# Optimization experiments

Hardware: AMD Instinct MI355X
Metric: run time of the kernel (lower is better)

Reference implementation:

```python
import jax, jax.numpy as jnp
import numpy as np

N = 50000   # nodes
E = 800000  # edges (avg degree 16)
F = 128     # input_nf = output_nf
H = 128     # hidden_nf


def setup_inputs() -> dict:
    key = jax.random.key(0)
    ks = jax.random.split(key, 10)
    # coords: spatial part in [-1, 1], z-coordinate (last dim) in [0.5, 1.5] (must be > 0)
    xz = jax.random.uniform(ks[0], (N, 3), minval=-1.0, maxval=1.0)
    xz = xz.at[:, -1].set(jax.random.uniform(ks[1], (N,), minval=0.5, maxval=1.5))
    h = jax.random.normal(ks[2], (N, F), dtype=jnp.float32)
    row = jax.random.randint(ks[3], (E,), 0, N)
    # guarantee col != row so AdS distance is strictly positive on every edge
    col = (row + 1 + jax.random.randint(ks[4], (E,), 0, N - 1)) % N
    edge_index = jnp.stack([row, col]).astype(jnp.int32)

    def lin(k, fan_in, fan_out):
        return jax.random.normal(k, (fan_in, fan_out), dtype=jnp.float32) / np.float32(np.sqrt(fan_in))

    return {
        "xz": xz,
        "h": h,
        "We1": lin(ks[5], 2 * F + 1, H), "be1": jnp.full((H,), 0.1, jnp.float32),
        "We2": lin(ks[6], H, H),         "be2": jnp.full((H,), 0.1, jnp.float32),
        "Wn1": lin(ks[7], H + F, H),     "bn1": jnp.full((H,), 0.1, jnp.float32),
        "Wn2": lin(ks[8], H, F),         "bn2": jnp.full((F,), 0.1, jnp.float32),
        "edge_index": edge_index,
    }


def reference(xz, h, We1, be1, We2, be2, Wn1, bn1, Wn2, bn2, edge_index):
    row, col = edge_index[0], edge_index[1]
    n = h.shape[0]

    # AdS (hyperbolic upper-half-space) distance between xz[row] and xz[col]:
    # d = arccosh(1 + |p1 - p2|^2 / (2 z1 z2)), z = last coordinate
    diff = xz[row] - xz[col]                                  # [E, 3]
    u = jnp.sum(diff * diff, axis=-1) / (2.0 * xz[row, -1] * xz[col, -1])
    dist = jnp.arccosh(1.0 + u)[:, None]                      # [E, 1]

    # edge model: concat(source, target, radial) -> Linear -> silu -> Linear -> silu
    m = jnp.concatenate([h[row], h[col], dist], axis=1)       # [E, 2F+1]
    m = jax.nn.silu(m @ We1 + be1)                            # [E, H]
    m = jax.nn.silu(m @ We2 + be2)                            # [E, H]

    # segment_mean over destination nodes (row)
    num = jax.ops.segment_sum(m, row, num_segments=n)                          # [N, H]
    den = jax.ops.segment_sum(jnp.ones_like(m), row, num_segments=n)          # [N, H]
    agg = num / jnp.maximum(den, jnp.ones((), den.dtype))

    # node model: concat(h, agg) -> Linear -> silu -> Linear, plus residual
    z = jnp.concatenate([h, agg], axis=1)                     # [N, F+H]
    out = jax.nn.silu(z @ Wn1 + bn1) @ Wn2 + bn2              # [N, F]
    return h + out
```

## Files before the change

### kernel.cpp

```cpp
#include <hip/hip_runtime.h>

#define NN 50000
#define EE 800000
#define NB 196

typedef __bf16 bf16x8 __attribute__((ext_vector_type(8)));
typedef float  f32x4  __attribute__((ext_vector_type(4)));

__device__ __forceinline__ float bf2f(ushort u) {
    union { unsigned int i; float f; } v; v.i = ((unsigned int)u) << 16; return v.f;
}
__device__ __forceinline__ ushort f2bf(float f) {
    union { float f; unsigned int i; } v; v.f = f;
    unsigned int u = v.i;
    return (ushort)((u + 0x7FFFu + ((u >> 16) & 1u)) >> 16);
}
__device__ __forceinline__ ushort f2bf_fast(float f) {
    union { float f; unsigned int i; } v; v.f = f;
    return (ushort)((v.i + 0x8000u) >> 16);
}
__device__ __forceinline__ float silu(float x) {
    return x * __builtin_amdgcn_rcpf(1.0f + __expf(-x));
}

__device__ __forceinline__ bool detect_isf(const ushort* __restrict__ xzu,
                                           int tid, int* scnt) {
    float v = bf2f(xzu[2 * (tid & 255)]);
    bool sane = (v == v) && (fabsf(v) <= 4.0f);
    unsigned long long m = __ballot(sane);
    if ((tid & 63) == 0) scnt[tid >> 6] = __popcll(m);
    __syncthreads();
    int cnt = scnt[0] + scnt[1] + scnt[2] + scnt[3];
    return cnt < 192;
}

__global__ void prep_all_kernel(const void* __restrict__ hsrc, const void* __restrict__ xzsrc,
                                const int* __restrict__ erow,
                                const void* We1, const void* We2,
                                const void* Wn1, const void* Wn2,
                                const void* be1, const void* be2,
                                const void* bn1, const void* bn2,
                                ushort* __restrict__ hb, float* __restrict__ xzf,
                                int* __restrict__ cntI,
                                ushort* __restrict__ We1s, ushort* __restrict__ We2s,
                                ushort* __restrict__ Wn1s, ushort* __restrict__ Wn2s,
                                float* __restrict__ fb, ushort* __restrict__ wlb) {
    __shared__ int scnt[4];
    const int b = blockIdx.x;
    const int tid = threadIdx.x;

    if (b >= 3712 && b < 6837) {
        int e = (b - 3712) * 256 + tid;
        if (e < EE) atomicAdd(&cntI[erow[e]], 1);
        return;
    }

    const bool isf = detect_isf((const ushort*)xzsrc, tid, scnt);

    if (b < 3125) {
        int i = (b * 256 + tid) * 8;
        uint4 o;
        if (isf) {
            const float* s = (const float*)hsrc + i;
            float4 f0 = *(const float4*)s;
            float4 f1 = *(const float4*)(s + 4);
            o.x = (unsigned int)f2bf(f0.x) | ((unsigned int)f2bf(f0.y) << 16);
            o.y = (unsigned int)f2bf(f0.z) | ((unsigned int)f2bf(f0.w) << 16);
            o.z = (unsigned int)f2bf(f1.x) | ((unsigned int)f2bf(f1.y) << 16);
            o.w = (unsigned int)f2bf(f1.z) | ((unsigned int)f2bf(f1.w) << 16);
        } else {
            o = *(const uint4*)((const ushort*)hsrc + i);
        }
        *(uint4*)(hb + i) = o;
    } else if (b < 3712) {
        int i = (b - 3125) * 256 + tid;
        if (i < NN * 3)
            xzf[i] = isf ? ((const float*)xzsrc)[i] : bf2f(((const ushort*)xzsrc)[i]);
    } else {
        int sw = b - 6837;
        if (sw == 48) {
            for (int j = tid; j < 640; j += 256) {
                int which = j >> 7, k = j & 127;
                const void* src = (which == 0) ? be1 : (which == 1) ? be2 :
                                  (which == 2) ? bn1 : (which == 3) ? bn2 : We1;
                size_t idx = (which == 4) ? ((size_t)256 * 128 + k) : (size_t)k;
                float v = isf ? ((const float*)src)[idx] : bf2f(((const ushort*)src)[idx]);
                fb[j] = v;
                if (which == 4) wlb[k] = f2bf(v);
            }
            return;
        }
        int c = sw * 256 + tid;
        const void* src; ushort* dst; int cl;
        if      (c <  4096) { src = We1; dst = We1s; cl = c;         }
        else if (c <  6144) { src = We2; dst = We2s; cl = c - 4096;  }
        else if (c < 10240) { src = Wn1; dst = Wn1s; cl = c - 6144;  }
        else                { src = Wn2; dst = Wn2s; cl = c - 10240; }
        int l = cl & 63, nt = (cl >> 6) & 7, kc = cl >> 9;
        int kbase = kc * 32 + (l >> 4) * 8;
        int n = nt * 16 + (l & 15);
        ushort tmp[8];
#pragma unroll
        for (int j = 0; j < 8; ++j) {
            size_t idx = (size_t)(kbase + j) * 128 + n;
            tmp[j] = isf ? f2bf(((const float*)src)[idx]) : ((const ushort*)src)[idx];
        }
#pragma unroll
        for (int j = 0; j < 8; ++j) dst[(size_t)cl * 8 + j] = tmp[j];
    }
}

__global__ void scanA_kernel(const int* __restrict__ cntI, int* __restrict__ bsum) {
    __shared__ int s[256];
    int t = threadIdx.x;
    int i = blockIdx.x * 256 + t;
    s[t] = (i < NN) ? cntI[i] : 0;
    __syncthreads();
#pragma unroll
    for (int off = 128; off > 0; off >>= 1) {
        if (t < off) s[t] += s[t + off];
        __syncthreads();
    }
    if (t == 0) bsum[blockIdx.x] = s[0];
}

__global__ void scanC_kernel(const int* __restrict__ cntI, const int* __restrict__ bsum,
                             int* __restrict__ rowStart) {
    __shared__ int s[256];
    __shared__ int sbase;
    int t = threadIdx.x;
    int bv = (t < NB) ? bsum[t] : 0;
    s[t] = bv;
    __syncthreads();
    for (int off = 1; off < 256; off <<= 1) {
        int u = (t >= off) ? s[t - off] : 0;
        __syncthreads();
        if (t >= off) s[t] += u;
        __syncthreads();
    }
    if (t == 0) sbase = (blockIdx.x == 0) ? 0 : s[blockIdx.x - 1];
    __syncthreads();
    int i = blockIdx.x * 256 + t;
    int v = (i < NN) ? cntI[i] : 0;
    s[t] = v;
    __syncthreads();
    for (int off = 1; off < 256; off <<= 1) {
        int u = (t >= off) ? s[t - off] : 0;
        __syncthreads();
        if (t >= off) s[t] += u;
        __syncthreads();
    }
    if (i < NN) rowStart[i] = sbase + s[t] - v;
}

__global__ __launch_bounds__(256, 3) void scatter_pq_kernel(
    const ushort* __restrict__ hb, const ushort* __restrict__ We1s,
    const float* __restrict__ fb, ushort* __restrict__ Pp, ushort* __restrict__ Qq,
    const int* __restrict__ erow, const int* __restrict__ ecol,
    const float* __restrict__ xzf, const int* __restrict__ rowStart,
    int* __restrict__ cursor, int4* __restrict__ eS) {
    __shared__ __align__(16) ushort sA[8192];
    const int tid = threadIdx.x;

    if (blockIdx.x >= 782) {
        int e = (blockIdx.x - 782) * 256 + tid;
        if (e >= EE) return;
        int r = erow[e], c = ecol[e];
        int pos = rowStart[r] + atomicAdd(&cursor[r], 1);
        float4 a = *(const float4*)(xzf + 3 * r);
        float4 b = *(const float4*)(xzf + 3 * c);
        float dx = a.x - b.x, dy = a.y - b.y, dz = a.z - b.z;
        float u = (dx * dx + dy * dy + dz * dz) * __builtin_amdgcn_rcpf(2.0f * a.z * b.z);
        u = fminf(fmaxf(u, 0.0f), 1.0e6f);
        float d = __logf(1.0f + u + sqrtf(u * (u + 2.0f)));
        eS[pos] = make_int4(r, c, __float_as_int(d), 0);
        return;
    }

    const int lane = tid & 63, w = tid >> 6;
    const int col = lane & 15, quad = lane >> 4;
    const int nt0 = w * 2;
    const int nA = w * 32 + col, nB = nA + 16;
    const float be1A = fb[nA], be1B = fb[nB];
    const int tile = blockIdx.x;
    const int n0 = tile * 64;
#pragma unroll
    for (int i = 0; i < 4; ++i) {
        int node = n0 + lane;
        uint4 v = (node < NN) ? *(const uint4*)(hb + (size_t)node * 128 + (w + 4 * i) * 8)
                              : make_uint4(0, 0, 0, 0);
        *(uint4*)(sA + (((lane >> 4) * 4 + i) * 64 + w * 16 + (lane & 15)) * 8) = v;
    }
    __syncthreads();

    f32x4 accP[4][2] = {}, accQ[4][2] = {};
#pragma unroll
    for (int kc = 0; kc < 4; ++kc) {
        bf16x8 bp0 = *(const bf16x8*)(We1s + ((kc * 8 + nt0)           * 64 + lane) * 8);
        bf16x8 bp1 = *(const bf16x8*)(We1s + ((kc * 8 + nt0 + 1)       * 64 + lane) * 8);
        bf16x8 bq0 = *(const bf16x8*)(We1s + (((kc + 4) * 8 + nt0)     * 64 + lane) * 8);
        bf16x8 bq1 = *(const bf16x8*)(We1s + (((kc + 4) * 8 + nt0 + 1) * 64 + lane) * 8);
#pragma unroll
        for (int g = 0; g < 4; ++g) {
            bf16x8 a = *(const bf16x8*)(sA + ((g * 4 + kc) * 64 + lane) * 8);
            accP[g][0] = __builtin_amdgcn_mfma_f32_16x16x32_bf16(a, bp0, accP[g][0], 0, 0, 0);
            accP[g][1] = __builtin_amdgcn_mfma_f32_16x16x32_bf16(a, bp1, accP[g][1], 0, 0, 0);
            accQ[g][0] = __builtin_amdgcn_mfma_f32_16x16x32_bf16(a, bq0, accQ[g][0], 0, 0, 0);
            accQ[g][1] = __builtin_amdgcn_mfma_f32_16x16x32_bf16(a, bq1, accQ[g][1], 0, 0, 0);
        }
    }
#pragma unroll
    for (int g = 0; g < 4; ++g) {
#pragma unroll
        for (int r = 0; r < 4; ++r) {
            int node = n0 + g * 16 + quad * 4 + r;
            if (node < NN) {
                size_t o = (size_t)node * 128;
                Pp[o + nA] = f2bf(accP[g][0][r] + be1A);
                Pp[o + nB] = f2bf(accP[g][1][r] + be1B);
                Qq[o + nA] = f2bf(accQ[g][0][r]);
                Qq[o + nB] = f2bf(accQ[g][1][r]);
            }
        }
    }
}

__global__ __launch_bounds__(256, 4) void edge_kernel(
    const ushort* __restrict__ Pp, const ushort* __restrict__ Qq,
    const int4* __restrict__ eS, const ushort* __restrict__ We2s,
    const ushort* __restrict__ wlb, const float* __restrict__ fb,
    float* __restrict__ agg) {
    __shared__ __align__(16) char smem[64 * 132 * 4];
    __shared__ int sRow[64];
    ushort* sM = (ushort*)smem;
    float (*sOut)[132] = (float(*)[132])smem;

    const int tid = threadIdx.x;
    const int lane = tid & 63, w = tid >> 6;
    const int col = lane & 15, quad = lane >> 4;
    const int nt0 = w * 2;

    const int nA = w * 32 + col, nB = nA + 16;
    const float be2A = fb[128 + nA], be2B = fb[128 + nB];

    const int ntiles = EE / 64;
    const int per = (ntiles + gridDim.x - 1) / gridDim.x;
    const int t0 = blockIdx.x * per;
    const int t1 = (t0 + per < ntiles) ? (t0 + per) : ntiles;
    if (t0 >= t1) return;

    bf16x8 B2[8];
#pragma unroll
    for (int kc = 0; kc < 4; ++kc) {
        B2[kc * 2]     = *(const bf16x8*)(We2s + ((kc * 8 + nt0)     * 64 + lane) * 8);
        B2[kc * 2 + 1] = *(const bf16x8*)(We2s + ((kc * 8 + nt0 + 1) * 64 + lane) * 8);
    }
    bf16x8 WL[4];
#pragma unroll
    for (int i = 0; i < 4; ++i) WL[i] = *(const bf16x8*)(wlb + (w + 4 * i) * 8);

    int4 ed = eS[(size_t)t0 * 64 + lane];

    for (int tile = t0; tile < t1; ++tile) {
        const int tn = (tile + 1 < t1) ? (tile + 1) : tile;
        const int4 edn = eS[(size_t)tn * 64 + lane];

        __syncthreads();
        const int r = ed.x, c = ed.y;
        const float d = __int_as_float(ed.z);
        if (w == 0) sRow[lane] = r;
#pragma unroll
        for (int i = 0; i < 4; ++i) {
            int ch = w + 4 * i;
            bf16x8 p = *(const bf16x8*)(Pp + (size_t)r * 128 + ch * 8);
            bf16x8 q = *(const bf16x8*)(Qq + (size_t)c * 128 + ch * 8);
            ushort out8[8];
#pragma unroll
            for (int j = 0; j < 8; ++j) {
                float x = (float)p[j] + (float)q[j] + d * (float)WL[i][j];
                out8[j] = f2bf_fast(silu(x));
            }
            *(uint4*)(sM + (((lane >> 4) * 4 + i) * 64 + w * 16 + (lane & 15)) * 8) =
                *(const uint4*)out8;
        }
        ed = edn;
        __syncthreads();

        f32x4 acc2[4][2] = {};
#pragma unroll
        for (int kc = 0; kc < 4; ++kc) {
#pragma unroll
            for (int g = 0; g < 4; ++g) {
                bf16x8 a = *(const bf16x8*)(sM + ((g * 4 + kc) * 64 + lane) * 8);
                acc2[g][0] = __builtin_amdgcn_mfma_f32_16x16x32_bf16(a, B2[kc * 2],     acc2[g][0], 0, 0, 0);
                acc2[g][1] = __builtin_amdgcn_mfma_f32_16x16x32_bf16(a, B2[kc * 2 + 1], acc2[g][1], 0, 0, 0);
            }
        }
        __syncthreads();

#pragma unroll
        for (int g = 0; g < 4; ++g) {
#pragma unroll
            for (int r4 = 0; r4 < 4; ++r4) {
                int m = g * 16 + quad * 4 + r4;
                sOut[m][nA] = silu(acc2[g][0][r4] + be2A);
                sOut[m][nB] = silu(acc2[g][1][r4] + be2B);
            }
        }
        __syncthreads();

        {
            const int cc = tid & 127;
            const int mb = (tid >> 7) * 32;
            float acc = 0.0f;
            int prow = sRow[mb];
            for (int k = 0; k < 32; ++k) {
                int rw = sRow[mb + k];
                if (rw != prow) {
                    unsafeAtomicAdd(&agg[(size_t)prow * 128 + cc], acc);
                    acc = 0.0f;
                    prow = rw;
                }
                acc += sOut[mb + k][cc];
            }
            unsafeAtomicAdd(&agg[(size_t)prow * 128 + cc], acc);
        }
    }
}

__global__ __launch_bounds__(256, 3) void node_kernel(
    const ushort* __restrict__ hb, const void* __restrict__ hraw,
    const void* __restrict__ xzsrc,
    const float* __restrict__ agg, const int* __restrict__ cntI,
    const ushort* __restrict__ Wn1s, const ushort* __restrict__ Wn2s,
    const float* __restrict__ fb, void* __restrict__ outv) {
    __shared__ __align__(16) ushort sA[16384];
    __shared__ __align__(16) ushort sM[8192];
    __shared__ int scnt[4];
    const int tid = threadIdx.x;
    const int lane = tid & 63, w = tid >> 6;
    const int col = lane & 15, quad = lane >> 4;
    const int nt0 = w * 2;
    const int ntiles = (NN + 63) / 64;
    const bool isf = detect_isf((const ushort*)xzsrc, tid, scnt);
    float* outf = (float*)outv;
    ushort* outu = (ushort*)outv;

    const int nA = w * 32 + col, nB = nA + 16;
    const float bn1A = fb[256 + nA], bn1B = fb[256 + nB];
    const float bn2A = fb[384 + nA], bn2B = fb[384 + nB];

    for (int tile = blockIdx.x; tile < ntiles; tile += gridDim.x) {
        __syncthreads();
        const int n0 = tile * 64;
#pragma unroll
        for (int i = 0; i < 8; ++i) {
            int kb = w + 4 * i;
            int node = n0 + lane;
            uint4 v;
            if (node < NN) {
                if (kb < 16) {
                    v = *(const uint4*)(hb + (size_t)node * 128 + kb * 8);
                } else {
                    const float* ap = agg + (size_t)node * 128 + (kb - 16) * 8;
                    float invc = __builtin_amdgcn_rcpf(fmaxf((float)cntI[node], 1.0f));
                    float4 f0 = *(const float4*)ap;
                    float4 f1 = *(const float4*)(ap + 4);
                    v.x = (unsigned int)f2bf_fast(f0.x * invc) | ((unsigned int)f2bf_fast(f0.y * invc) << 16);
                    v.y = (unsigned int)f2bf_fast(f0.z * invc) | ((unsigned int)f2bf_fast(f0.w * invc) << 16);
                    v.z = (unsigned int)f2bf_fast(f1.x * invc) | ((unsigned int)f2bf_fast(f1.y * invc) << 16);
                    v.w = (unsigned int)f2bf_fast(f1.z * invc) | ((unsigned int)f2bf_fast(f1.w * invc) << 16);
                }
            } else {
                v = make_uint4(0, 0, 0, 0);
            }
            *(uint4*)(sA + (((quad * 8 + i) * 64) + w * 16 + col) * 8) = v;
        }
        __syncthreads();

        f32x4 acc[4][2] = {};
#pragma unroll
        for (int kc = 0; kc < 8; ++kc) {
            bf16x8 b0 = *(const bf16x8*)(Wn1s + ((kc * 8 + nt0)     * 64 + lane) * 8);
            bf16x8 b1 = *(const bf16x8*)(Wn1s + ((kc * 8 + nt0 + 1) * 64 + lane) * 8);
#pragma unroll
            for (int g = 0; g < 4; ++g) {
                bf16x8 a = *(const bf16x8*)(sA + ((g * 8 + kc) * 64 + lane) * 8);
                acc[g][0] = __builtin_amdgcn_mfma_f32_16x16x32_bf16(a, b0, acc[g][0], 0, 0, 0);
                acc[g][1] = __builtin_amdgcn_mfma_f32_16x16x32_bf16(a, b1, acc[g][1], 0, 0, 0);
            }
        }
#pragma unroll
        for (int g = 0; g < 4; ++g) {
            int base0 = ((g * 4 + w) * 64 + (col >> 3) * 16) * 8 + (col & 7);
#pragma unroll
            for (int r = 0; r < 4; ++r) {
                int mrow = quad * 4 + r;
                sM[base0 + mrow * 8]              = f2bf_fast(silu(acc[g][0][r] + bn1A));
                sM[base0 + 2 * 16 * 8 + mrow * 8] = f2bf_fast(silu(acc[g][1][r] + bn1B));
            }
        }
        __syncthreads();

        f32x4 acc2[4][2] = {};
#pragma unroll
        for (int kc = 0; kc < 4; ++kc) {
            bf16x8 b0 = *(const bf16x8*)(Wn2s + ((kc * 8 + nt0)     * 64 + lane) * 8);
            bf16x8 b1 = *(const bf16x8*)(Wn2s + ((kc * 8 + nt0 + 1) * 64 + lane) * 8);
#pragma unroll
            for (int g = 0; g < 4; ++g) {
                bf16x8 a = *(const bf16x8*)(sM + ((g * 4 + kc) * 64 + lane) * 8);
                acc2[g][0] = __builtin_amdgcn_mfma_f32_16x16x32_bf16(a, b0, acc2[g][0], 0, 0, 0);
                acc2[g][1] = __builtin_amdgcn_mfma_f32_16x16x32_bf16(a, b1, acc2[g][1], 0, 0, 0);
            }
        }
#pragma unroll
        for (int g = 0; g < 4; ++g) {
#pragma unroll
            for (int r = 0; r < 4; ++r) {
                int ml2 = g * 16 + quad * 4 + r;
                int node = n0 + ml2;
                if (node < NN) {
                    size_t oi = (size_t)node * 128;
                    float h0 = isf ? ((const float*)hraw)[oi + nA] : bf2f(((const ushort*)hraw)[oi + nA]);
                    float h1 = isf ? ((const float*)hraw)[oi + nB] : bf2f(((const ushort*)hraw)[oi + nB]);
                    float x0 = acc2[g][0][r] + bn2A + h0;
                    float x1 = acc2[g][1][r] + bn2B + h1;
                    if (isf) { outf[oi + nA] = x0; outf[oi + nB] = x1; }
                    else     { outu[oi + nA] = f2bf_fast(x0); outu[oi + nB] = f2bf_fast(x1); }
                }
            }
        }
    }
}

extern "C" void kernel_launch(void* const* d_in, const int* in_sizes, int n_in,
                              void* d_out, int out_size, void* d_ws, size_t ws_size,
                              hipStream_t stream) {
    const void* xz  = d_in[0];
    const void* h   = d_in[1];
    const void* We1 = d_in[2];
    const void* be1 = d_in[3];
    const void* We2 = d_in[4];
    const void* be2 = d_in[5];
    const void* Wn1 = d_in[6];
    const void* bn1 = d_in[7];
    const void* Wn2 = d_in[8];
    const void* bn2 = d_in[9];
    const int*  ei  = (const int*)d_in[10];
    const int* erow = ei;
    const int* ecol = ei + EE;

    char* base = (char*)d_ws;
    size_t cur = 0;
    auto alloc = [&](size_t bytes) { size_t o = cur; cur = (cur + bytes + 255) & ~(size_t)255; return o; };
    float*  agg    = (float*) (base + alloc((size_t)NN * 128 * 4));
    int*    cntI   = (int*)   (base + alloc((size_t)NN * 4));
    int*    cursor = (int*)   (base + alloc((size_t)NN * 4));
    ushort* hb     = (ushort*)(base + alloc((size_t)NN * 128 * 2));
    ushort* Pp     = (ushort*)(base + alloc((size_t)NN * 128 * 2));
    ushort* Qq     = (ushort*)(base + alloc((size_t)NN * 128 * 2));
    int4*   eS     = (int4*)  (base + alloc((size_t)EE * 16));
    float*  xzf    = (float*) (base + alloc((size_t)NN * 3 * 4 + 16));
    int*    rowSt  = (int*)   (base + alloc((size_t)NN * 4));
    int*    bsum   = (int*)   (base + alloc(256 * 4));
    ushort* We1s   = (ushort*)(base + alloc(32768 * 2));
    ushort* We2s   = (ushort*)(base + alloc(16384 * 2));
    ushort* Wn1s   = (ushort*)(base + alloc(32768 * 2));
    ushort* Wn2s   = (ushort*)(base + alloc(16384 * 2));
    float*  fb     = (float*) (base + alloc(640 * 4));
    ushort* wlb    = (ushort*)(base + alloc(128 * 2));

    size_t zbytes = (size_t)((char*)hb - (char*)agg);
    (void)hipMemsetAsync(agg, 0, zbytes, stream);

    prep_all_kernel<<<6886, 256, 0, stream>>>(h, xz, erow, We1, We2, Wn1, Wn2,
                                              be1, be2, bn1, bn2,
                                              hb, xzf, cntI, We1s, We2s, Wn1s, Wn2s,
                                              fb, wlb);
    scanA_kernel<<<NB, 256, 0, stream>>>(cntI, bsum);
    scanC_kernel<<<NB, 256, 0, stream>>>(cntI, bsum, rowSt);
    scatter_pq_kernel<<<782 + 3125, 256, 0, stream>>>(hb, We1s, fb, Pp, Qq,
                                                      erow, ecol, xzf, rowSt, cursor, eS);
    edge_kernel<<<1024, 256, 0, stream>>>(Pp, Qq, eS, We2s, wlb, fb, agg);
    node_kernel<<<782, 256, 0, stream>>>(hb, h, xz, agg, cntI, Wn1s, Wn2s, fb, d_out);
}
```

Baseline: 331.8 us.

## Software-pipeline edge kernel with double-buffered message tile and gather prefetch

The edge kernel gets a double-buffered shared-memory tile for the first-layer activations, and the P/Q gathers for the next tile are issued before the current tile's MFMA work. Gather latency can then overlap with compute, and one barrier per tile is removed. In exchange, shared memory grows because sM and sOut no longer alias, more registers hold the prefetched data, and launch bounds drop from 4 to 2 blocks per CU, which lowers occupancy.

```diff
diff --git a/kernel.cpp b/kernel.cpp
--- a/kernel.cpp
+++ b/kernel.cpp
@@ -225,15 +225,14 @@
     }
 }
 
-__global__ __launch_bounds__(256, 4) void edge_kernel(
+__global__ __launch_bounds__(256, 2) void edge_kernel(
     const ushort* __restrict__ Pp, const ushort* __restrict__ Qq,
     const int4* __restrict__ eS, const ushort* __restrict__ We2s,
     const ushort* __restrict__ wlb, const float* __restrict__ fb,
     float* __restrict__ agg) {
-    __shared__ __align__(16) char smem[64 * 132 * 4];
+    __shared__ __align__(16) ushort sM[2][8192];
+    __shared__ __align__(16) float sOut[64][132];
     __shared__ int sRow[64];
-    ushort* sM = (ushort*)smem;
-    float (*sOut)[132] = (float(*)[132])smem;
 
     const int tid = threadIdx.x;
     const int lane = tid & 63, w = tid >> 6;
@@ -249,55 +248,63 @@
     const int t1 = (t0 + per < ntiles) ? (t0 + per) : ntiles;
     if (t0 >= t1) return;
 
-    bf16x8 B2[8];
+    bf16x8 B2r[8];
 #pragma unroll
     for (int kc = 0; kc < 4; ++kc) {
-        B2[kc * 2]     = *(const bf16x8*)(We2s + ((kc * 8 + nt0)     * 64 + lane) * 8);
-        B2[kc * 2 + 1] = *(const bf16x8*)(We2s + ((kc * 8 + nt0 + 1) * 64 + lane) * 8);
+        B2r[kc * 2]     = *(const bf16x8*)(We2s + ((kc * 8 + nt0)     * 64 + lane) * 8);
+        B2r[kc * 2 + 1] = *(const bf16x8*)(We2s + ((kc * 8 + nt0 + 1) * 64 + lane) * 8);
     }
     bf16x8 WL[4];
 #pragma unroll
     for (int i = 0; i < 4; ++i) WL[i] = *(const bf16x8*)(wlb + (w + 4 * i) * 8);
 
     int4 ed = eS[(size_t)t0 * 64 + lane];
-
-    for (int tile = t0; tile < t1; ++tile) {
-        const int tn = (tile + 1 < t1) ? (tile + 1) : tile;
-        const int4 edn = eS[(size_t)tn * 64 + lane];
-
-        __syncthreads();
-        const int r = ed.x, c = ed.y;
+    int4 edn = eS[(size_t)((t0 + 1 < t1) ? t0 + 1 : t0) * 64 + lane];
+    {
         const float d = __int_as_float(ed.z);
-        if (w == 0) sRow[lane] = r;
 #pragma unroll
         for (int i = 0; i < 4; ++i) {
-            int ch = w + 4 * i;
-            bf16x8 p = *(const bf16x8*)(Pp + (size_t)r * 128 + ch * 8);
-            bf16x8 q = *(const bf16x8*)(Qq + (size_t)c * 128 + ch * 8);
+            bf16x8 p = *(const bf16x8*)(Pp + (size_t)ed.x * 128 + (w + 4 * i) * 8);
+            bf16x8 q = *(const bf16x8*)(Qq + (size_t)ed.y * 128 + (w + 4 * i) * 8);
             ushort out8[8];
 #pragma unroll
             for (int j = 0; j < 8; ++j) {
                 float x = (float)p[j] + (float)q[j] + d * (float)WL[i][j];
                 out8[j] = f2bf_fast(silu(x));
             }
-            *(uint4*)(sM + (((lane >> 4) * 4 + i) * 64 + w * 16 + (lane & 15)) * 8) =
+            *(uint4*)(&sM[0][(((lane >> 4) * 4 + i) * 64 + w * 16 + (lane & 15)) * 8]) =
                 *(const uint4*)out8;
         }
-        ed = edn;
-        __syncthreads();
+    }
+    int cur = 0;
+
+    for (int tile = t0; tile < t1; ++tile) {
+        const bool haveNext = (tile + 1 < t1);
+        __syncthreads();
+
+        const int tnn = (tile + 2 < t1) ? tile + 2 : t1 - 1;
+        const int4 ednn = eS[(size_t)tnn * 64 + lane];
+
+        bf16x8 p[4], q[4];
+        if (haveNext) {
+#pragma unroll
+            for (int i = 0; i < 4; ++i) {
+                p[i] = *(const bf16x8*)(Pp + (size_t)edn.x * 128 + (w + 4 * i) * 8);
+                q[i] = *(const bf16x8*)(Qq + (size_t)edn.y * 128 + (w + 4 * i) * 8);
+            }
+        }
+        if (w == 0) sRow[lane] = ed.x;
 
         f32x4 acc2[4][2] = {};
 #pragma unroll
         for (int kc = 0; kc < 4; ++kc) {
 #pragma unroll
             for (int g = 0; g < 4; ++g) {
-                bf16x8 a = *(const bf16x8*)(sM + ((g * 4 + kc) * 64 + lane) * 8);
-                acc2[g][0] = __builtin_amdgcn_mfma_f32_16x16x32_bf16(a, B2[kc * 2],     acc2[g][0], 0, 0, 0);
-                acc2[g][1] = __builtin_amdgcn_mfma_f32_16x16x32_bf16(a, B2[kc * 2 + 1], acc2[g][1], 0, 0, 0);
-            }
-        }
-        __syncthreads();
-
+                bf16x8 a = *(const bf16x8*)(&sM[cur][((g * 4 + kc) * 64 + lane) * 8]);
+                acc2[g][0] = __builtin_amdgcn_mfma_f32_16x16x32_bf16(a, B2r[kc * 2],     acc2[g][0], 0, 0, 0);
+                acc2[g][1] = __builtin_amdgcn_mfma_f32_16x16x32_bf16(a, B2r[kc * 2 + 1], acc2[g][1], 0, 0, 0);
+            }
+        }
 #pragma unroll
         for (int g = 0; g < 4; ++g) {
 #pragma unroll
@@ -305,6 +312,20 @@
                 int m = g * 16 + quad * 4 + r4;
                 sOut[m][nA] = silu(acc2[g][0][r4] + be2A);
                 sOut[m][nB] = silu(acc2[g][1][r4] + be2B);
+            }
+        }
+        if (haveNext) {
+            const float d = __int_as_float(edn.z);
+#pragma unroll
+            for (int i = 0; i < 4; ++i) {
+                ushort out8[8];
+#pragma unroll
+                for (int j = 0; j < 8; ++j) {
+                    float x = (float)p[i][j] + (float)q[i][j] + d * (float)WL[i][j];
+                    out8[j] = f2bf_fast(silu(x));
+                }
+                *(uint4*)(&sM[cur ^ 1][(((lane >> 4) * 4 + i) * 64 + w * 16 + (lane & 15)) * 8]) =
+                    *(const uint4*)out8;
             }
         }
         __syncthreads();
@@ -325,6 +346,7 @@
             }
             unsafeAtomicAdd(&agg[(size_t)prow * 128 + cc], acc);
         }
+        ed = edn; edn = ednn; cur ^= 1;
     }
 }
 
```

Result: slower. 342.3 us (+3.2%).
